# Kernel tuning notes

Hardware: AMD Instinct MI355X
Metric: run time of the kernel (lower is better)

The kernel has to match this reference:

```python
import jax, jax.numpy as jnp
import numpy as np

N_NODES = 100000


def sage_conv(x, src, dst, w_self, w_neigh, b):
    # DGL SAGEConv with 'mean' aggregator: out = x @ W_self + mean_neigh(x) @ W_neigh + b
    msg = x[src]                                                     # [E, d] gather
    agg = jax.ops.segment_sum(msg, dst, num_segments=N_NODES)        # [N, d]
    deg = jax.ops.segment_sum(jnp.ones((src.shape[0],), x.dtype), dst,
                              num_segments=N_NODES)                  # [N]
    h_neigh = agg / jnp.maximum(deg, 1.0)[:, None]                   # mean; 0 for isolated nodes
    return x @ w_self + h_neigh @ w_neigh + b


def setup_inputs() -> dict:
    key = jax.random.key(0)
    ks = jax.random.split(key, 12)
    N, E = N_NODES, 1600000
    in_f, h_f, r_f = 128, 128, 64
    glorot = lambda k, i, o: jax.random.normal(k, (i, o), jnp.float32) / np.float32(np.sqrt(i))
    return {
        "in_feat": jax.random.normal(ks[0], (N, in_f), jnp.float32),
        "src": jax.random.randint(ks[1], (E,), 0, N),
        "dst": jax.random.randint(ks[2], (E,), 0, N),
        "w1_self": glorot(ks[3], in_f, h_f), "w1_neigh": glorot(ks[4], in_f, h_f), "b1": jnp.zeros((h_f,), jnp.float32),
        "w2_self": glorot(ks[5], h_f, r_f), "w2_neigh": glorot(ks[6], h_f, r_f), "b2": jnp.zeros((r_f,), jnp.float32),
        "w3_self": glorot(ks[7], r_f, r_f), "w3_neigh": glorot(ks[8], r_f, r_f), "b3": jnp.zeros((r_f,), jnp.float32),
    }


def reference(in_feat, src, dst,
              w1_self, w1_neigh, b1,
              w2_self, w2_neigh, b2,
              w3_self, w3_neigh, b3):
    h = sage_conv(in_feat, src, dst, w1_self, w1_neigh, b1)
    h = jax.nn.relu(h)
    h = sage_conv(h, src, dst, w2_self, w2_neigh, b2)
    h = jax.nn.relu(h)
    # dropout is treated as identity (deterministic eval-mode reference)
    h = sage_conv(h, src, dst, w3_self, w3_neigh, b3)
    return jax.nn.softmax(h, axis=-1)
```

## Files before the change

### kernel.cpp

```cpp
#include <hip/hip_runtime.h>
#include <hip/hip_bf16.h>

#define N_NODES 100000

typedef unsigned short ushort_t;
typedef __attribute__((ext_vector_type(8))) short short8;
typedef __attribute__((ext_vector_type(4))) float f32x4;

static __device__ __forceinline__ ushort_t f2bf(float f) {
    unsigned u = __float_as_uint(f);
    unsigned r = u + 0x7FFFu + ((u >> 16) & 1u);
    return (ushort_t)(r >> 16);
}
static __device__ __forceinline__ float bf2f(ushort_t h) {
    return __uint_as_float(((unsigned)h) << 16);
}

static __device__ __forceinline__ void split8(const float* __restrict__ xp,
                                              short8& hi, short8& lo) {
    float4 x0 = *(const float4*)xp;
    float4 x1 = *(const float4*)(xp + 4);
    float xs[8] = {x0.x, x0.y, x0.z, x0.w, x1.x, x1.y, x1.z, x1.w};
    #pragma unroll
    for (int j = 0; j < 8; ++j) {
        ushort_t h = f2bf(xs[j]);
        hi[j] = (short)h;
        lo[j] = (short)f2bf(xs[j] - bf2f(h));
    }
}

__global__ __launch_bounds__(256) void hist_kernel(const int* __restrict__ dst,
                                                   int* __restrict__ deg, int E) {
    int e = blockIdx.x * 256 + threadIdx.x;
    if (e < E) atomicAdd(&deg[dst[e]], 1);
}

__global__ __launch_bounds__(256) void scan_partial_sums(const int* __restrict__ deg,
                                                         int* __restrict__ partials, int N) {
    __shared__ int wsums[4];
    int tid = threadIdx.x, lane = tid & 63, wv = tid >> 6;
    int i0 = blockIdx.x * 1024 + tid * 4;
    int s = 0;
    #pragma unroll
    for (int j = 0; j < 4; ++j) {
        int i = i0 + j;
        if (i < N) s += deg[i];
    }
    #pragma unroll
    for (int off = 32; off > 0; off >>= 1) s += __shfl_xor(s, off, 64);
    if (lane == 0) wsums[wv] = s;
    __syncthreads();
    if (tid == 0)
        partials[blockIdx.x] = wsums[0] + wsums[1] + wsums[2] + wsums[3];
}

__global__ __launch_bounds__(256) void scan_partials(int* __restrict__ partials, int NB,
                                                     int* __restrict__ row_ptr, int N) {
    __shared__ int wsums[4];
    int tid = threadIdx.x, lane = tid & 63, wv = tid >> 6;
    int v = (tid < NB) ? partials[tid] : 0;
    int x = v;
    #pragma unroll
    for (int off = 1; off < 64; off <<= 1) {
        int y = __shfl_up(x, off, 64);
        if (lane >= off) x += y;
    }
    if (lane == 63) wsums[wv] = x;
    __syncthreads();
    int woff = 0;
    for (int w = 0; w < wv; ++w) woff += wsums[w];
    int incl = x + woff;
    if (tid < NB) partials[tid] = incl - v;
    if (tid == NB - 1) row_ptr[N] = incl;
}

__global__ __launch_bounds__(256) void scan_emit(const int* __restrict__ deg,
                                                 const int* __restrict__ partials,
                                                 int* __restrict__ row_ptr,
                                                 int* __restrict__ cursor,
                                                 float* __restrict__ inv_deg, int N) {
    __shared__ int wsums[4];
    int tid = threadIdx.x, lane = tid & 63, wv = tid >> 6;
    int i0 = blockIdx.x * 1024 + tid * 4;
    int d[4];
    #pragma unroll
    for (int j = 0; j < 4; ++j) {
        int i = i0 + j;
        d[j] = (i < N) ? deg[i] : 0;
    }
    int s = d[0] + d[1] + d[2] + d[3];
    int x = s;
    #pragma unroll
    for (int off = 1; off < 64; off <<= 1) {
        int y = __shfl_up(x, off, 64);
        if (lane >= off) x += y;
    }
    if (lane == 63) wsums[wv] = x;
    __syncthreads();
    int woff = 0;
    for (int w = 0; w < wv; ++w) woff += wsums[w];
    int run = partials[blockIdx.x] + woff + x - s;
    #pragma unroll
    for (int j = 0; j < 4; ++j) {
        int i = i0 + j;
        if (i < N) {
            row_ptr[i] = run;
            cursor[i]  = run;
            inv_deg[i] = 1.0f / (float)(d[j] > 0 ? d[j] : 1);
            run += d[j];
        }
    }
}

__global__ __launch_bounds__(256) void fill_kernel(const int* __restrict__ src,
                                                   const int* __restrict__ dst,
                                                   int* __restrict__ cursor,
                                                   int* __restrict__ edge_src, int E) {
    int e = blockIdx.x * 256 + threadIdx.x;
    if (e < E) {
        int d = dst[e];
        int p = atomicAdd(&cursor[d], 1);
        edge_src[p] = src[e];
    }
}

__global__ __launch_bounds__(256) void pack_w(const float* __restrict__ W,
                                              ushort_t* __restrict__ Hi,
                                              ushort_t* __restrict__ Lo,
                                              int K, int NS) {
    int tid = blockIdx.x * 256 + threadIdx.x;
    int total = (K * NS) / 8;
    if (tid >= total) return;
    int l  = tid & 63;
    int fl = tid >> 6;
    int NT = NS / 16;
    int t = fl % NT, s = fl / NT;
    ushort_t hs[8], ls[8];
    #pragma unroll
    for (int j = 0; j < 8; ++j) {
        int k = s * 32 + (l >> 4) * 8 + j;
        int n = t * 16 + (l & 15);
        float w = W[(size_t)k * NS + n];
        ushort_t h = f2bf(w);
        hs[j] = h;
        ls[j] = f2bf(w - bf2f(h));
    }
    #pragma unroll
    for (int j = 0; j < 8; ++j) {
        Hi[(size_t)tid * 8 + j] = hs[j];
        Lo[(size_t)tid * 8 + j] = ls[j];
    }
}

template <int K, int NS>
__global__ __launch_bounds__(256) void mfma_gemm(const float* __restrict__ X,
                                                 const ushort_t* __restrict__ BsHi,
                                                 const ushort_t* __restrict__ BsLo,
                                                 const ushort_t* __restrict__ BnHi,
                                                 const ushort_t* __restrict__ BnLo,
                                                 const float* __restrict__ bias,
                                                 float* __restrict__ S,
                                                 ushort_t* __restrict__ Zb,
                                                 int M) {
    constexpr int KS = K / 32;
    constexpr int NT = NS / 16;
    int tid = threadIdx.x;
    int lane = tid & 63, w = tid >> 6;
    int baseM = blockIdx.x * 128 + w * 32;
    int rIn = lane & 15, q = lane >> 4;

    short8 Ahi[KS][2], Alo[KS][2];
    #pragma unroll
    for (int s = 0; s < KS; ++s) {
        #pragma unroll
        for (int mt = 0; mt < 2; ++mt) {
            int gm = baseM + mt * 16 + rIn;
            if (gm < M) {
                split8(&X[(size_t)gm * K + s * 32 + q * 8], Ahi[s][mt], Alo[s][mt]);
            } else {
                #pragma unroll
                for (int j = 0; j < 8; ++j) { Ahi[s][mt][j] = 0; Alo[s][mt][j] = 0; }
            }
        }
    }

    for (int t = 0; t < NT; ++t) {
        f32x4 aS0 = {0.f, 0.f, 0.f, 0.f}, aS1 = {0.f, 0.f, 0.f, 0.f};
        f32x4 aZ0 = {0.f, 0.f, 0.f, 0.f}, aZ1 = {0.f, 0.f, 0.f, 0.f};
        #pragma unroll
        for (int s = 0; s < KS; ++s) {
            size_t fo = ((size_t)(s * NT + t) * 64 + lane) * 8;
            short8 bsh = *(const short8*)&BsHi[fo];
            short8 bsl = *(const short8*)&BsLo[fo];
            short8 bnh = *(const short8*)&BnHi[fo];
            short8 bnl = *(const short8*)&BnLo[fo];
            aS0 = __builtin_amdgcn_mfma_f32_16x16x32_bf16(Ahi[s][0], bsh, aS0, 0, 0, 0);
            aS0 = __builtin_amdgcn_mfma_f32_16x16x32_bf16(Alo[s][0], bsh, aS0, 0, 0, 0);
            aS0 = __builtin_amdgcn_mfma_f32_16x16x32_bf16(Ahi[s][0], bsl, aS0, 0, 0, 0);
            aS1 = __builtin_amdgcn_mfma_f32_16x16x32_bf16(Ahi[s][1], bsh, aS1, 0, 0, 0);
            aS1 = __builtin_amdgcn_mfma_f32_16x16x32_bf16(Alo[s][1], bsh, aS1, 0, 0, 0);
            aS1 = __builtin_amdgcn_mfma_f32_16x16x32_bf16(Ahi[s][1], bsl, aS1, 0, 0, 0);
            aZ0 = __builtin_amdgcn_mfma_f32_16x16x32_bf16(Ahi[s][0], bnh, aZ0, 0, 0, 0);
            aZ0 = __builtin_amdgcn_mfma_f32_16x16x32_bf16(Alo[s][0], bnh, aZ0, 0, 0, 0);
            aZ0 = __builtin_amdgcn_mfma_f32_16x16x32_bf16(Ahi[s][0], bnl, aZ0, 0, 0, 0);
            aZ1 = __builtin_amdgcn_mfma_f32_16x16x32_bf16(Ahi[s][1], bnh, aZ1, 0, 0, 0);
            aZ1 = __builtin_amdgcn_mfma_f32_16x16x32_bf16(Alo[s][1], bnh, aZ1, 0, 0, 0);
            aZ1 = __builtin_amdgcn_mfma_f32_16x16x32_bf16(Ahi[s][1], bnl, aZ1, 0, 0, 0);
        }
        int col = t * 16 + rIn;
        float bv = bias[col];
        #pragma unroll
        for (int mt = 0; mt < 2; ++mt) {
            f32x4 aS = mt ? aS1 : aS0;
            f32x4 aZ = mt ? aZ1 : aZ0;
            #pragma unroll
            for (int r = 0; r < 4; ++r) {
                int gm = baseM + mt * 16 + q * 4 + r;
                if (gm < M) {
                    S[(size_t)gm * NS + col]  = aS[r] + bv;
                    Zb[(size_t)gm * NS + col] = f2bf(aZ[r]);
                }
            }
        }
    }
}

template <int D, int ACT>
__global__ __launch_bounds__(256) void agg_kernel(const float* __restrict__ S,
                                                  const uint2* __restrict__ Zu,
                                                  const int* __restrict__ row_ptr,
                                                  const int* __restrict__ edge_src,
                                                  const float* __restrict__ inv_deg,
                                                  float* __restrict__ out, int N) {
    constexpr int G  = D / 4;
    constexpr int NG = 256 / G;
    int tid = threadIdx.x;
    int g = tid / G, f4 = tid % G;
    int n = blockIdx.x * NG + g;
    if (n >= N) return;
    int beg = row_ptr[n], end = row_ptr[n + 1];

    float a0[4] = {0, 0, 0, 0}, a1[4] = {0, 0, 0, 0};
    float a2[4] = {0, 0, 0, 0}, a3[4] = {0, 0, 0, 0};
#define ACC(u, a)                                                              \
    a[0] += __uint_as_float((u).x << 16);                                      \
    a[1] += __uint_as_float((u).x & 0xFFFF0000u);                              \
    a[2] += __uint_as_float((u).y << 16);                                      \
    a[3] += __uint_as_float((u).y & 0xFFFF0000u);
    int j = beg;
    for (; j + 3 < end; j += 4) {
        int s0 = edge_src[j + 0], s1 = edge_src[j + 1];
        int s2 = edge_src[j + 2], s3 = edge_src[j + 3];
        uint2 u0 = Zu[(size_t)s0 * G + f4];
        uint2 u1 = Zu[(size_t)s1 * G + f4];
        uint2 u2 = Zu[(size_t)s2 * G + f4];
        uint2 u3 = Zu[(size_t)s3 * G + f4];
        ACC(u0, a0) ACC(u1, a1) ACC(u2, a2) ACC(u3, a3)
    }
    for (; j < end; ++j) {
        uint2 u = Zu[(size_t)edge_src[j] * G + f4];
        ACC(u, a0)
    }
#undef ACC
    float id = inv_deg[n];
    float4 sv = ((const float4*)(S + (size_t)n * D))[f4];
    float v[4];
    v[0] = sv.x + id * ((a0[0] + a1[0]) + (a2[0] + a3[0]));
    v[1] = sv.y + id * ((a0[1] + a1[1]) + (a2[1] + a3[1]));
    v[2] = sv.z + id * ((a0[2] + a1[2]) + (a2[2] + a3[2]));
    v[3] = sv.w + id * ((a0[3] + a1[3]) + (a2[3] + a3[3]));

    float4 o;
    if (ACT == 0) {
        o.x = fmaxf(v[0], 0.f); o.y = fmaxf(v[1], 0.f);
        o.z = fmaxf(v[2], 0.f); o.w = fmaxf(v[3], 0.f);
    } else {
        float m = fmaxf(fmaxf(v[0], v[1]), fmaxf(v[2], v[3]));
        #pragma unroll
        for (int off = 8; off > 0; off >>= 1) m = fmaxf(m, __shfl_xor(m, off, 16));
        float e0 = __expf(v[0] - m), e1 = __expf(v[1] - m);
        float e2 = __expf(v[2] - m), e3 = __expf(v[3] - m);
        float s = (e0 + e1) + (e2 + e3);
        #pragma unroll
        for (int off = 8; off > 0; off >>= 1) s += __shfl_xor(s, off, 16);
        float inv = 1.0f / s;
        o.x = e0 * inv; o.y = e1 * inv; o.z = e2 * inv; o.w = e3 * inv;
    }
    ((float4*)(out + (size_t)n * D))[f4] = o;
}

extern "C" void kernel_launch(void* const* d_in, const int* in_sizes, int n_in,
                              void* d_out, int out_size, void* d_ws, size_t ws_size,
                              hipStream_t stream) {
    const float* in_feat = (const float*)d_in[0];
    const int*   src     = (const int*)d_in[1];
    const int*   dst     = (const int*)d_in[2];
    const float* w1s = (const float*)d_in[3];
    const float* w1n = (const float*)d_in[4];
    const float* b1  = (const float*)d_in[5];
    const float* w2s = (const float*)d_in[6];
    const float* w2n = (const float*)d_in[7];
    const float* b2  = (const float*)d_in[8];
    const float* w3s = (const float*)d_in[9];
    const float* w3n = (const float*)d_in[10];
    const float* b3  = (const float*)d_in[11];

    const int N = N_NODES;
    const int E = in_sizes[1];

    char* p = (char*)d_ws;
    auto carve = [&](size_t bytes) -> char* {
        char* q = p;
        p += (bytes + 511) & ~(size_t)511;
        return q;
    };
    float*    S        = (float*)   carve((size_t)N * 128 * sizeof(float));
    ushort_t* Zb       = (ushort_t*)carve((size_t)N * 128 * sizeof(ushort_t));
    float*    H        = (float*)   carve((size_t)N * 128 * sizeof(float));
    int*      edge_src = (int*)     carve((size_t)E * sizeof(int));
    int*      row_ptr  = (int*)     carve((size_t)(N + 1) * sizeof(int));
    int*      cursor   = (int*)     carve((size_t)N * sizeof(int));
    int*      deg      = (int*)     carve((size_t)N * sizeof(int));
    float*    invd     = (float*)   carve((size_t)N * sizeof(float));
    int*      partials = (int*)     carve(256 * sizeof(int));
    ushort_t* P1sH = (ushort_t*)carve(128 * 128 * 2); ushort_t* P1sL = (ushort_t*)carve(128 * 128 * 2);
    ushort_t* P1nH = (ushort_t*)carve(128 * 128 * 2); ushort_t* P1nL = (ushort_t*)carve(128 * 128 * 2);
    ushort_t* P2sH = (ushort_t*)carve(128 * 64 * 2);  ushort_t* P2sL = (ushort_t*)carve(128 * 64 * 2);
    ushort_t* P2nH = (ushort_t*)carve(128 * 64 * 2);  ushort_t* P2nL = (ushort_t*)carve(128 * 64 * 2);
    ushort_t* P3sH = (ushort_t*)carve(64 * 64 * 2);   ushort_t* P3sL = (ushort_t*)carve(64 * 64 * 2);
    ushort_t* P3nH = (ushort_t*)carve(64 * 64 * 2);   ushort_t* P3nL = (ushort_t*)carve(64 * 64 * 2);

    pack_w<<<(128 * 128 / 8 + 255) / 256, 256, 0, stream>>>(w1s, P1sH, P1sL, 128, 128);
    pack_w<<<(128 * 128 / 8 + 255) / 256, 256, 0, stream>>>(w1n, P1nH, P1nL, 128, 128);
    pack_w<<<(128 * 64 / 8 + 255) / 256, 256, 0, stream>>>(w2s, P2sH, P2sL, 128, 64);
    pack_w<<<(128 * 64 / 8 + 255) / 256, 256, 0, stream>>>(w2n, P2nH, P2nL, 128, 64);
    pack_w<<<(64 * 64 / 8 + 255) / 256, 256, 0, stream>>>(w3s, P3sH, P3sL, 64, 64);
    pack_w<<<(64 * 64 / 8 + 255) / 256, 256, 0, stream>>>(w3n, P3nH, P3nL, 64, 64);

    hipMemsetAsync(deg, 0, (size_t)N * sizeof(int), stream);
    hist_kernel<<<(E + 255) / 256, 256, 0, stream>>>(dst, deg, E);
    const int NB = (N + 1023) / 1024;
    scan_partial_sums<<<NB, 256, 0, stream>>>(deg, partials, N);
    scan_partials<<<1, 256, 0, stream>>>(partials, NB, row_ptr, N);
    scan_emit<<<NB, 256, 0, stream>>>(deg, partials, row_ptr, cursor, invd, N);
    fill_kernel<<<(E + 255) / 256, 256, 0, stream>>>(src, dst, cursor, edge_src, E);

    const int GB = (N + 127) / 128;

    mfma_gemm<128, 128><<<GB, 256, 0, stream>>>(in_feat, P1sH, P1sL, P1nH, P1nL, b1, S, Zb, N);
    agg_kernel<128, 0><<<(N + 7) / 8, 256, 0, stream>>>(S, (const uint2*)Zb,
                                                        row_ptr, edge_src, invd, H, N);

    mfma_gemm<128, 64><<<GB, 256, 0, stream>>>(H, P2sH, P2sL, P2nH, P2nL, b2, S, Zb, N);
    agg_kernel<64, 0><<<(N + 15) / 16, 256, 0, stream>>>(S, (const uint2*)Zb,
                                                         row_ptr, edge_src, invd, H, N);

    mfma_gemm<64, 64><<<GB, 256, 0, stream>>>(H, P3sH, P3sL, P3nH, P3nL, b3, S, Zb, N);
    agg_kernel<64, 1><<<(N + 15) / 16, 256, 0, stream>>>(S, (const uint2*)Zb,
                                                         row_ptr, edge_src, invd,
                                                         (float*)d_out, N);
}
```

Baseline: 564.8 us.

## Partition CSR fill by destination range and merge weight-pack launches

The edge-fill scatter becomes 8 groups of 128 blocks. Each group scans every edge but only places those whose destination falls in its 1/8 node range, so the scattered atomics and edge_src writes of a group cover a narrower address window, which should help cache locality. The price is reading dst eight times. The six weight-packing launches are also merged into one 28-block kernel to cut launch overhead.

```diff
diff --git a/kernel.cpp b/kernel.cpp
--- a/kernel.cpp
+++ b/kernel.cpp
@@ -112,25 +112,44 @@
     }
 }
 
-__global__ __launch_bounds__(256) void fill_kernel(const int* __restrict__ src,
-                                                   const int* __restrict__ dst,
-                                                   int* __restrict__ cursor,
-                                                   int* __restrict__ edge_src, int E) {
-    int e = blockIdx.x * 256 + threadIdx.x;
-    if (e < E) {
+#define FILL_GROUPS 8
+#define FILL_BPG    128
+__global__ __launch_bounds__(256) void fill_part(const int* __restrict__ src,
+                                                 const int* __restrict__ dst,
+                                                 int* __restrict__ cursor,
+                                                 int* __restrict__ edge_src,
+                                                 int E, int N) {
+    int g    = blockIdx.x & (FILL_GROUPS - 1);
+    int bInG = blockIdx.x >> 3;
+    int lo = (int)((long long)N * g / FILL_GROUPS);
+    int hi = (int)((long long)N * (g + 1) / FILL_GROUPS);
+    int stride = FILL_BPG * 256;
+    for (int e = bInG * 256 + threadIdx.x; e < E; e += stride) {
         int d = dst[e];
-        int p = atomicAdd(&cursor[d], 1);
-        edge_src[p] = src[e];
-    }
-}
-
-__global__ __launch_bounds__(256) void pack_w(const float* __restrict__ W,
-                                              ushort_t* __restrict__ Hi,
-                                              ushort_t* __restrict__ Lo,
-                                              int K, int NS) {
-    int tid = blockIdx.x * 256 + threadIdx.x;
-    int total = (K * NS) / 8;
-    if (tid >= total) return;
+        if (d >= lo && d < hi) {
+            int p = atomicAdd(&cursor[d], 1);
+            edge_src[p] = src[e];
+        }
+    }
+}
+
+__global__ __launch_bounds__(256) void pack_all(
+        const float* __restrict__ W0, const float* __restrict__ W1,
+        const float* __restrict__ W2, const float* __restrict__ W3,
+        const float* __restrict__ W4, const float* __restrict__ W5,
+        ushort_t* H0, ushort_t* L0, ushort_t* H1, ushort_t* L1,
+        ushort_t* H2, ushort_t* L2, ushort_t* H3, ushort_t* L3,
+        ushort_t* H4, ushort_t* L4, ushort_t* H5, ushort_t* L5) {
+    int b = blockIdx.x;
+    const float* W; ushort_t* Hi; ushort_t* Lo; int K, NS, base;
+    if (b < 8)       { W = W0; Hi = H0; Lo = L0; K = 128; NS = 128; base = 0;  }
+    else if (b < 16) { W = W1; Hi = H1; Lo = L1; K = 128; NS = 128; base = 8;  }
+    else if (b < 20) { W = W2; Hi = H2; Lo = L2; K = 128; NS = 64;  base = 16; }
+    else if (b < 24) { W = W3; Hi = H3; Lo = L3; K = 128; NS = 64;  base = 20; }
+    else if (b < 26) { W = W4; Hi = H4; Lo = L4; K = 64;  NS = 64;  base = 24; }
+    else             { W = W5; Hi = H5; Lo = L5; K = 64;  NS = 64;  base = 26; }
+    int tid = (b - base) * 256 + threadIdx.x;
+    if (tid >= (K * NS) / 8) return;
     int l  = tid & 63;
     int fl = tid >> 6;
     int NT = NS / 16;
@@ -330,12 +349,10 @@
     ushort_t* P3sH = (ushort_t*)carve(64 * 64 * 2);   ushort_t* P3sL = (ushort_t*)carve(64 * 64 * 2);
     ushort_t* P3nH = (ushort_t*)carve(64 * 64 * 2);   ushort_t* P3nL = (ushort_t*)carve(64 * 64 * 2);
 
-    pack_w<<<(128 * 128 / 8 + 255) / 256, 256, 0, stream>>>(w1s, P1sH, P1sL, 128, 128);
-    pack_w<<<(128 * 128 / 8 + 255) / 256, 256, 0, stream>>>(w1n, P1nH, P1nL, 128, 128);
-    pack_w<<<(128 * 64 / 8 + 255) / 256, 256, 0, stream>>>(w2s, P2sH, P2sL, 128, 64);
-    pack_w<<<(128 * 64 / 8 + 255) / 256, 256, 0, stream>>>(w2n, P2nH, P2nL, 128, 64);
-    pack_w<<<(64 * 64 / 8 + 255) / 256, 256, 0, stream>>>(w3s, P3sH, P3sL, 64, 64);
-    pack_w<<<(64 * 64 / 8 + 255) / 256, 256, 0, stream>>>(w3n, P3nH, P3nL, 64, 64);
+    pack_all<<<28, 256, 0, stream>>>(w1s, w1n, w2s, w2n, w3s, w3n,
+                                     P1sH, P1sL, P1nH, P1nL,
+                                     P2sH, P2sL, P2nH, P2nL,
+                                     P3sH, P3sL, P3nH, P3nL);
 
     hipMemsetAsync(deg, 0, (size_t)N * sizeof(int), stream);
     hist_kernel<<<(E + 255) / 256, 256, 0, stream>>>(dst, deg, E);
@@ -343,7 +360,7 @@
     scan_partial_sums<<<NB, 256, 0, stream>>>(deg, partials, N);
     scan_partials<<<1, 256, 0, stream>>>(partials, NB, row_ptr, N);
     scan_emit<<<NB, 256, 0, stream>>>(deg, partials, row_ptr, cursor, invd, N);
-    fill_kernel<<<(E + 255) / 256, 256, 0, stream>>>(src, dst, cursor, edge_src, E);
+    fill_part<<<FILL_GROUPS * FILL_BPG, 256, 0, stream>>>(src, dst, cursor, edge_src, E, N);
 
     const int GB = (N + 127) / 128;
 
```

New measurement: 520.3 us. 1.09x faster.
